# Performance work log

Hardware: AMD Instinct MI355X
Metric: run time of the kernel (lower is better)

The kernel has to match this reference:

```python
import jax, jax.numpy as jnp
import numpy as np

NUM_CLASSES = 91
NUM_ANCHORS = 3234
VAR_XY, VAR_WH = 0.1, 0.2
SCORE_THRESH = 0.05
NMS_THRESH = 0.5
PRE_NMS_TOPK = 200  # original default 400; reduced to bound the [C-1,K,K] IoU buffer
MAX_DET = 100
BATCH = 64


def _xyxy_to_cxcywh(b):
    wh = b[..., 2:] - b[..., :2]
    c = b[..., :2] + 0.5 * wh
    return jnp.concatenate([c, wh], axis=-1)


def _pairwise_iou(b):
    # b: [K,4] xyxy -> [K,K] IoU
    lt = jnp.maximum(b[:, None, :2], b[None, :, :2])
    rb = jnp.minimum(b[:, None, 2:], b[None, :, 2:])
    inter = jnp.prod(jnp.clip(rb - lt, 0.0), axis=-1)
    area = jnp.prod(jnp.clip(b[:, 2:] - b[:, :2], 0.0), axis=-1)
    union = area[:, None] + area[None, :] - inter
    return inter / jnp.maximum(union, 1e-9)


def _nms_keep(boxes):
    # boxes [K,4] already sorted by descending score; greedy NMS keep mask [K]
    K = boxes.shape[0]
    iou = _pairwise_iou(jax.lax.stop_gradient(boxes))
    idx = jnp.arange(K)

    def body(i, keep):
        suppress = keep[i] & (iou[i] > NMS_THRESH) & (idx > i)
        return keep & ~suppress

    return jax.lax.fori_loop(0, K, body, jnp.ones((K,), dtype=bool))


def setup_inputs() -> dict:
    key = jax.random.key(0)
    k1, k2, k3, k4 = jax.random.split(key, 4)
    cls_logits = jax.random.normal(k1, (BATCH, NUM_ANCHORS, NUM_CLASSES), dtype=jnp.float32)
    box_reg = jax.random.normal(k2, (BATCH, NUM_ANCHORS, 4), dtype=jnp.float32)
    # valid normalized anchor boxes in xyxy
    cxy = jax.random.uniform(k3, (NUM_ANCHORS, 2), minval=0.05, maxval=0.95)
    wh = jax.random.uniform(k4, (NUM_ANCHORS, 2), minval=0.02, maxval=0.4)
    priors = jnp.concatenate([cxy - wh / 2, cxy + wh / 2], axis=-1).astype(jnp.float32)
    return {"cls_logits": cls_logits, "box_reg": box_reg, "priors": priors}


def reference(cls_logits, box_reg, priors):
    probs = jax.nn.softmax(cls_logits, axis=-1)           # [B,A,C]
    pr_c = _xyxy_to_cxcywh(priors)                        # [A,4]

    def per_image(args):
        loc, p = args                                     # [A,4], [A,C]
        # _decode with variances (0.1, 0.2)
        xy = loc[:, :2] * VAR_XY * pr_c[:, 2:] + pr_c[:, :2]
        wh = jnp.exp(loc[:, 2:] * VAR_WH) * pr_c[:, 2:]
        boxes = jnp.concatenate([xy - wh / 2, xy + wh / 2], axis=-1)  # [A,4]

        scores_c = p[:, 1:].T                             # [C-1, A], skip background
        vals, idx = jax.lax.top_k(scores_c, PRE_NMS_TOPK)  # [C-1,K] sorted desc
        boxes_c = boxes[idx]                              # [C-1,K,4]
        keep = jax.vmap(_nms_keep)(boxes_c)               # [C-1,K]
        valid = vals > SCORE_THRESH
        fscores = jnp.where(keep & valid, vals, 0.0)      # masked-out dets scored 0
        labels = jnp.broadcast_to(
            jnp.arange(1, NUM_CLASSES, dtype=jnp.float32)[:, None], fscores.shape)

        flat_s = fscores.reshape(-1)
        flat_b = boxes_c.reshape(-1, 4)
        flat_l = labels.reshape(-1)
        top_s, top_i = jax.lax.top_k(flat_s, MAX_DET)     # global top-100 by score
        preds = jnp.concatenate(
            [flat_b[top_i], top_s[:, None], flat_l[top_i, None]], axis=-1)  # [100,6]
        return jnp.where(top_s[:, None] > 0, preds, 0.0)  # zero padding rows

    return jax.lax.map(per_image, (box_reg, probs))        # [B,100,6]
```

## Files before the change

kernel.cpp:

```cpp
#include <hip/hip_runtime.h>
#include <cstdint>

#define NCLS 91
#define NA   3234
#define NB   64
#define KTOP 200
#define CAP  128
#define MAXDET 100
#define NCM1 90
#define CAPI 8192
#define LCAP 256
#define NBIN 1024
#define BOFF 0x3D4C
#define FBUF 1024
#define PBLK 6468

typedef unsigned long long u64;
typedef unsigned int u32;


__device__ __forceinline__ u64 u64max(u64 a, u64 b) { return a > b ? a : b; }
__device__ __forceinline__ u64 u64min(u64 a, u64 b) { return a < b ? a : b; }

__device__ __forceinline__ u64 shfl_xor_u64(u64 v, int m) {
  int lo = __shfl_xor((int)(u32)v, m, 64);
  int hi = __shfl_xor((int)(u32)(v >> 32), m, 64);
  return ((u64)(u32)hi << 32) | (u32)lo;
}

template <int SLOTS>
__device__ __forceinline__ void bitonic_desc(u64* key, int t) {
  const int N = SLOTS * 64;
  for (int k = 2; k <= N; k <<= 1) {
    for (int j = k >> 1; j > 0; j >>= 1) {
      if (j >= 64) {
        int sj = j >> 6;
        #pragma unroll
        for (int s = 0; s < SLOTS; ++s) {
          int sp = s ^ sj;
          if (sp > s) {
            int e = s * 64 + t;
            bool up = ((e & k) == 0);
            u64 a = key[s], b = key[sp];
            u64 mx = u64max(a, b), mn = u64min(a, b);
            key[s]  = up ? mx : mn;
            key[sp] = up ? mn : mx;
          }
        }
      } else {
        #pragma unroll
        for (int s = 0; s < SLOTS; ++s) {
          int e = s * 64 + t;
          u64 p = shfl_xor_u64(key[s], j);
          bool up = ((e & k) == 0);
          bool lower = ((t & j) == 0);
          key[s] = (up == lower) ? u64max(key[s], p) : u64min(key[s], p);
        }
      }
    }
  }
}

__device__ __forceinline__ void process_slab(
    const float* sl, int slab, int t,
    u64* lkey, unsigned short* lbc, int* lcnt) {
  int half = t & 1;
  int r = t >> 1;
  int i = slab * 32 + r;
  int b = i / NA, a = i - b * NA;

  int F0 = half ? 45 : 0;
  int cntf = half ? 46 : 45;
  const float* base = sl + r * 91 + F0;
  int g0 = (int)((u32)(r * 91 + F0) & 3u);
  int lead = (4 - g0) & 3;
  int rem = cntf - lead;
  int n4 = rem >> 2;
  int tail = rem & 3;

  float lv0 = 0.f, lv1 = 0.f, lv2 = 0.f;
  if (lead > 0) lv0 = base[0];
  if (lead > 1) lv1 = base[1];
  if (lead > 2) lv2 = base[2];
  const float4* cv = (const float4*)(base + lead);
  float4 r4[11];
  #pragma unroll
  for (int v = 0; v < 10; ++v) r4[v] = cv[v];
  r4[10] = make_float4(0.f, 0.f, 0.f, 0.f);
  if (n4 > 10) r4[10] = cv[10];
  int toff = lead + 4 * n4;
  float tv0 = 0.f, tv1 = 0.f, tv2 = 0.f;
  if (tail > 0) tv0 = base[toff];
  if (tail > 1) tv1 = base[toff + 1];
  if (tail > 2) tv2 = base[toff + 2];

  float m = -3.402823466e38f;
  if (lead > 0) m = fmaxf(m, lv0);
  if (lead > 1) m = fmaxf(m, lv1);
  if (lead > 2) m = fmaxf(m, lv2);
  #pragma unroll
  for (int v = 0; v < 10; ++v) {
    float4 q = r4[v];
    m = fmaxf(m, fmaxf(fmaxf(q.x, q.y), fmaxf(q.z, q.w)));
  }
  if (n4 > 10) {
    float4 q = r4[10];
    m = fmaxf(m, fmaxf(fmaxf(q.x, q.y), fmaxf(q.z, q.w)));
  }
  if (tail > 0) m = fmaxf(m, tv0);
  if (tail > 1) m = fmaxf(m, tv1);
  if (tail > 2) m = fmaxf(m, tv2);
  m = fmaxf(m, __shfl_xor(m, 1, 64));

  float el0 = expf(lv0 - m), el1 = expf(lv1 - m), el2 = expf(lv2 - m);
  float4 er[11];
  #pragma unroll
  for (int v = 0; v < 11; ++v) {
    er[v].x = expf(r4[v].x - m);
    er[v].y = expf(r4[v].y - m);
    er[v].z = expf(r4[v].z - m);
    er[v].w = expf(r4[v].w - m);
  }
  float et0 = expf(tv0 - m), et1 = expf(tv1 - m), et2 = expf(tv2 - m);

  auto CHAIN = [&](float s) -> float {
    if (lead > 0) s += el0;
    if (lead > 1) s += el1;
    if (lead > 2) s += el2;
    #pragma unroll
    for (int v = 0; v < 10; ++v) {
      s += er[v].x; s += er[v].y; s += er[v].z; s += er[v].w;
    }
    if (n4 > 10) { s += er[10].x; s += er[10].y; s += er[10].z; s += er[10].w; }
    if (tail > 0) s += et0;
    if (tail > 1) s += et1;
    if (tail > 2) s += et2;
    return s;
  };
  float s = 0.f;
  if (!half) s = CHAIN(0.f);
  float s_recv = __shfl_xor(s, 1, 64);
  if (half) s = CHAIN(s_recv);
  float fin = __shfl_xor(s, 1, 64);
  float ssum = half ? s : fin;

  float lthr = logf(0.05f * ssum);
  u64 abits = (u64)(u32)(~a);
  int bb90 = b * NCM1;
  #define PUSH(L, E, CC) do { \
    if ((L) - m > lthr) { \
      float _e = (E); \
      int _lp = atomicAdd(lcnt, 1); \
      if (_lp < LCAP) { \
        lkey[_lp] = ((u64)__float_as_uint(_e / ssum) << 32) | abits; \
        lbc[_lp] = (unsigned short)(bb90 + (CC) - 1); \
      } \
    } \
  } while (0)

  if (lead > 0 && F0 != 0) PUSH(lv0, el0, F0);
  if (lead > 1) PUSH(lv1, el1, F0 + 1);
  if (lead > 2) PUSH(lv2, el2, F0 + 2);
  {
    int c0 = F0 + lead;
    if (c0 != 0) PUSH(r4[0].x, er[0].x, c0);
    PUSH(r4[0].y, er[0].y, c0 + 1);
    PUSH(r4[0].z, er[0].z, c0 + 2);
    PUSH(r4[0].w, er[0].w, c0 + 3);
  }
  #pragma unroll
  for (int v = 1; v < 10; ++v) {
    int cb = F0 + lead + 4 * v;
    PUSH(r4[v].x, er[v].x, cb);
    PUSH(r4[v].y, er[v].y, cb + 1);
    PUSH(r4[v].z, er[v].z, cb + 2);
    PUSH(r4[v].w, er[v].w, cb + 3);
  }
  if (n4 > 10) {
    int cb = F0 + lead + 40;
    PUSH(r4[10].x, er[10].x, cb);
    PUSH(r4[10].y, er[10].y, cb + 1);
    PUSH(r4[10].z, er[10].z, cb + 2);
    PUSH(r4[10].w, er[10].w, cb + 3);
  }
  {
    int cb = F0 + toff;
    if (tail > 0) PUSH(tv0, et0, cb);
    if (tail > 1) PUSH(tv1, et1, cb + 1);
    if (tail > 2) PUSH(tv2, et2, cb + 2);
  }
  #undef PUSH
}

__global__ __launch_bounds__(64, 2) void prep_kernel(
    const float* __restrict__ logits, const float* __restrict__ box_reg,
    const float* __restrict__ priors, float* __restrict__ boxes,
    u64* __restrict__ cand, int* __restrict__ cnt) {
  __shared__ __align__(16) float sl[2912];
  __shared__ u64 lkey[LCAP];
  __shared__ unsigned short lbc[LCAP];
  __shared__ int lcnt;
  int t = threadIdx.x;
  if (t == 0) lcnt = 0;
  asm volatile("s_waitcnt lgkmcnt(0)" ::: "memory");

  int half = t & 1;
  int rloc = t >> 1;
  int i = blockIdx.x * 32 + rloc;
  int b = i / NA, a = i - b * NA;

  float4 pr = make_float4(0.f, 0.f, 0.f, 0.f);
  float4 lc = make_float4(0.f, 0.f, 0.f, 0.f);
  if (!half) {
    pr = ((const float4*)priors)[a];
    lc = ((const float4*)box_reg)[i];
  }

  const float4* gs = (const float4*)(logits + (size_t)blockIdx.x * 2912);
  float4 v0  = gs[0 * 64 + t];
  float4 v1  = gs[1 * 64 + t];
  float4 v2  = gs[2 * 64 + t];
  float4 v3  = gs[3 * 64 + t];
  float4 v4  = gs[4 * 64 + t];
  float4 v5  = gs[5 * 64 + t];
  float4 v6  = gs[6 * 64 + t];
  float4 v7  = gs[7 * 64 + t];
  float4 v8  = gs[8 * 64 + t];
  float4 v9  = gs[9 * 64 + t];
  float4 v10 = gs[10 * 64 + t];
  bool lastl = (t < 24);
  float4 v11 = make_float4(0.f, 0.f, 0.f, 0.f);
  if (lastl) v11 = gs[11 * 64 + t];

  if (!half) {
    float pw = pr.z - pr.x, ph = pr.w - pr.y;
    float cx = pr.x + 0.5f * pw, cy = pr.y + 0.5f * ph;
    float x = lc.x * 0.1f * pw + cx;
    float y = lc.y * 0.1f * ph + cy;
    float bw = expf(lc.z * 0.2f) * pw;
    float bh = expf(lc.w * 0.2f) * ph;
    float4 bxo;
    bxo.x = x - bw * 0.5f; bxo.y = y - bh * 0.5f;
    bxo.z = x + bw * 0.5f; bxo.w = y + bh * 0.5f;
    ((float4*)boxes)[i] = bxo;
  }

  float4* sl4 = (float4*)sl;
  sl4[0 * 64 + t]  = v0;
  sl4[1 * 64 + t]  = v1;
  sl4[2 * 64 + t]  = v2;
  sl4[3 * 64 + t]  = v3;
  sl4[4 * 64 + t]  = v4;
  sl4[5 * 64 + t]  = v5;
  sl4[6 * 64 + t]  = v6;
  sl4[7 * 64 + t]  = v7;
  sl4[8 * 64 + t]  = v8;
  sl4[9 * 64 + t]  = v9;
  sl4[10 * 64 + t] = v10;
  if (lastl) sl4[11 * 64 + t] = v11;

  asm volatile("s_waitcnt lgkmcnt(0)" ::: "memory");
  __builtin_amdgcn_sched_barrier(0);

  process_slab(sl, blockIdx.x, t, lkey, lbc, &lcnt);

  asm volatile("s_waitcnt lgkmcnt(0)" ::: "memory");
  __builtin_amdgcn_sched_barrier(0);
  int nL = lcnt; if (nL > LCAP) nL = LCAP;
  for (int j = t; j < nL; j += 64) {
    int bcv = lbc[j];
    int pos = atomicAdd(&cnt[bcv], 1);
    if (pos < CAP) cand[(size_t)bcv * CAP + pos] = lkey[j];
  }
}

__global__ __launch_bounds__(256) void sort_nms_kernel(
    const u64* __restrict__ cand, const int* __restrict__ cnt,
    const float* __restrict__ boxes,
    u64* __restrict__ img_keys, int* __restrict__ img_cnt) {
  int w = threadIdx.x >> 6;
  int t = threadIdx.x & 63;
  int bc = blockIdx.x * 4 + w;
  int b = bc / NCM1;
  int cm1 = bc - b * NCM1;

  int n = cnt[bc]; if (n > CAP) n = CAP;

  u64 key[2];
  #pragma unroll
  for (int s = 0; s < 2; ++s) {
    int e = s * 64 + t;
    key[s] = (e < n) ? cand[(size_t)bc * CAP + e] : 0ULL;
  }
  if (n <= 64) bitonic_desc<1>(key, t);
  else         bitonic_desc<2>(key, t);

  float4 bx0 = make_float4(0.f, 0.f, 0.f, 0.f);
  float4 bx1 = make_float4(0.f, 0.f, 0.f, 0.f);
  float ar0 = 0.f, ar1 = 0.f;
  if (t < n) {
    int a = (int)(~(u32)key[0]);
    bx0 = ((const float4*)boxes)[b * NA + a];
    ar0 = fmaxf(bx0.z - bx0.x, 0.f) * fmaxf(bx0.w - bx0.y, 0.f);
  }
  if (64 + t < n) {
    int a = (int)(~(u32)key[1]);
    bx1 = ((const float4*)boxes)[b * NA + a];
    ar1 = fmaxf(bx1.z - bx1.x, 0.f) * fmaxf(bx1.w - bx1.y, 0.f);
  }

  auto rng = [](int mm, int wd) -> u64 {
    int c = mm - wd * 64;
    if (c <= 0) return 0ull;
    if (c >= 64) return ~0ull;
    return (1ull << c) - 1ull;
  };
  u64 kp0 = rng(n, 0), kp1 = rng(n, 1);
  bool has1 = (n > 64);

  for (int i = 0; i < n; ++i) {
    bool hi = i >= 64;
    u64 kw = hi ? kp1 : kp0;
    if (!((kw >> (i & 63)) & 1ull)) continue;
    int src = i & 63;
    float bix = __shfl(hi ? bx1.x : bx0.x, src, 64);
    float biy = __shfl(hi ? bx1.y : bx0.y, src, 64);
    float biz = __shfl(hi ? bx1.z : bx0.z, src, 64);
    float biw = __shfl(hi ? bx1.w : bx0.w, src, 64);
    float ai  = __shfl(hi ? ar1 : ar0, src, 64);
    if (!hi) {
      float xx1 = fmaxf(bix, bx0.x), yy1 = fmaxf(biy, bx0.y);
      float xx2 = fminf(biz, bx0.z), yy2 = fminf(biw, bx0.w);
      float inter = fmaxf(xx2 - xx1, 0.f) * fmaxf(yy2 - yy1, 0.f);
      float iou = inter / fmaxf(ai + ar0 - inter, 1e-9f);
      u64 sup0 = __ballot(iou > 0.5f);
      kp0 &= ~(sup0 & ~((2ull << i) - 1ull));
      if (has1) {
        float xx1b = fmaxf(bix, bx1.x), yy1b = fmaxf(biy, bx1.y);
        float xx2b = fminf(biz, bx1.z), yy2b = fminf(biw, bx1.w);
        float interb = fmaxf(xx2b - xx1b, 0.f) * fmaxf(yy2b - yy1b, 0.f);
        float ioub = interb / fmaxf(ai + ar1 - interb, 1e-9f);
        u64 sup1 = __ballot(ioub > 0.5f);
        kp1 &= ~sup1;
      }
    } else {
      float xx1b = fmaxf(bix, bx1.x), yy1b = fmaxf(biy, bx1.y);
      float xx2b = fminf(biz, bx1.z), yy2b = fminf(biw, bx1.w);
      float interb = fmaxf(xx2b - xx1b, 0.f) * fmaxf(yy2b - yy1b, 0.f);
      float ioub = interb / fmaxf(ai + ar1 - interb, 1e-9f);
      u64 sup1 = __ballot(ioub > 0.5f);
      kp1 &= ~(sup1 & ~((2ull << (i - 64)) - 1ull));
    }
  }

  u64 k0 = kp0, k1 = kp1;
  int c0 = __popcll(k0), c1 = __popcll(k1);
  int tot = c0 + c1;
  int base = 0;
  if (t == 0 && tot) base = atomicAdd(&img_cnt[b], tot);
  base = __shfl(base, 0, 64);
  if (tot) {
    u64 lmlt = (1ull << t) - 1ull;
    u64 kws[2] = {k0, k1};
    int pres[2] = {0, c0};
    #pragma unroll
    for (int s = 0; s < 2; ++s) {
      int rr = s * 64 + t;
      if (rr < n && ((kws[s] >> t) & 1ull)) {
        int pos = base + pres[s] + __popcll(kws[s] & lmlt);
        if (pos < CAPI) {
          u32 sbits = (u32)(key[s] >> 32);
          int fidx = cm1 * KTOP + rr;
          int anch = (int)(~(u32)key[s]);
          img_keys[(size_t)b * CAPI + pos] =
              ((u64)sbits << 27) | ((u64)(u32)(0x7FFF - fidx) << 12) | (u64)(u32)anch;
        }
      }
    }
  }
}

__global__ __launch_bounds__(1024) void topdet_kernel(
    const u64* __restrict__ img_keys, const int* __restrict__ img_cnt,
    const float* __restrict__ boxes, float* __restrict__ out) {
  __shared__ int hist[NBIN];
  __shared__ u64 buf[FBUF];
  __shared__ int sh_nsel, sh_T;
  int b = blockIdx.x, t = threadIdx.x;
  int n = img_cnt[b]; if (n > CAPI) n = CAPI;

  for (int i = t; i < NBIN; i += 1024) hist[i] = 0;
  if (t == 0) { sh_nsel = 0; sh_T = 0; }
  __syncthreads();

  for (int i = t; i < n; i += 1024) {
    int bin = (int)(img_keys[(size_t)b * CAPI + i] >> 43) - BOFF;
    bin = bin < 0 ? 0 : (bin > NBIN - 1 ? NBIN - 1 : bin);
    atomicAdd(&hist[bin], 1);
  }
  __syncthreads();

  if (t < 64) {
    int hi = NBIN - 1 - (t << 4);
    int cs = 0;
    #pragma unroll
    for (int k = 0; k < 16; ++k) cs += hist[hi - k];
    int cum = cs;
    for (int d = 1; d < 64; d <<= 1) {
      int o = __shfl_up(cum, d, 64);
      if (t >= d) cum += o;
    }
    int pre = cum - cs;
    if (pre < MAXDET && cum >= MAXDET) {
      int acc = pre;
      for (int k = 0; k < 16; ++k) {
        acc += hist[hi - k];
        if (acc >= MAXDET) { sh_T = hi - k; break; }
      }
    }
  }
  __syncthreads();

  int T = sh_T;
  for (int i = t; i < n; i += 1024) {
    u64 key = img_keys[(size_t)b * CAPI + i];
    int bin = (int)(key >> 43) - BOFF;
    bin = bin < 0 ? 0 : (bin > NBIN - 1 ? NBIN - 1 : bin);
    if (bin >= T) {
      int pos = atomicAdd(&sh_nsel, 1);
      if (pos < FBUF) buf[pos] = key;
    }
  }
  __syncthreads();

  int ns = sh_nsel; if (ns > FBUF) ns = FBUF;

  if (ns <= 256) {
    if (t < 64) {
      u64 key[4];
      #pragma unroll
      for (int s = 0; s < 4; ++s) {
        int e = s * 64 + t;
        key[s] = (e < ns) ? buf[e] : 0ULL;
      }
      if (ns <= 128) bitonic_desc<2>(key, t);
      else           bitonic_desc<4>(key, t);
      buf[t] = key[0];
      if (t < 36) buf[64 + t] = key[1];
    }
    __syncthreads();
  } else {
    int npow = 1; while (npow < ns) npow <<= 1;
    for (int i = t; i < npow; i += 1024) if (i >= ns) buf[i] = 0ULL;
    __syncthreads();
    for (int k = 2; k <= npow; k <<= 1) {
      for (int j = k >> 1; j > 0; j >>= 1) {
        for (int i = t; i < npow; i += 1024) {
          int l = i ^ j;
          if (l > i) {
            u64 x0 = buf[i], x1 = buf[l];
            bool up = ((i & k) == 0);
            if (up ? (x0 < x1) : (x0 > x1)) { buf[i] = x1; buf[l] = x0; }
          }
        }
        __syncthreads();
      }
    }
  }

  if (t < MAXDET) {
    float* row = out + ((size_t)b * MAXDET + t) * 6;
    if (t < ns) {
      u64 key = buf[t];
      float vsc = __uint_as_float((u32)(key >> 27));
      int fidx = 0x7FFF - (int)((key >> 12) & 0x7FFF);
      int a = (int)(key & 0xFFF);
      float4 bb = ((const float4*)boxes)[b * NA + a];
      row[0] = bb.x; row[1] = bb.y; row[2] = bb.z; row[3] = bb.w;
      row[4] = vsc;
      row[5] = (float)(fidx / KTOP + 1);
    } else {
      row[0] = 0.f; row[1] = 0.f; row[2] = 0.f;
      row[3] = 0.f; row[4] = 0.f; row[5] = 0.f;
    }
  }
}

extern "C" void kernel_launch(void* const* d_in, const int* in_sizes, int n_in,
                              void* d_out, int out_size, void* d_ws, size_t ws_size,
                              hipStream_t stream) {
  const float* logits  = (const float*)d_in[0];
  const float* box_reg = (const float*)d_in[1];
  const float* priors  = (const float*)d_in[2];
  float* out = (float*)d_out;

  char* ws = (char*)d_ws;
  size_t off = 0;
  float* boxes = (float*)(ws + off);               off += (size_t)NB * NA * 4 * sizeof(float);
  u64* cand = (u64*)(ws + off);                    off += (size_t)NB * NCM1 * CAP * sizeof(u64);
  u64* img_keys = (u64*)(ws + off);                off += (size_t)NB * CAPI * sizeof(u64);
  int* cnt = (int*)(ws + off);                     off += (size_t)NB * NCM1 * sizeof(int);
  int* img_cnt = (int*)(ws + off);                 off += (size_t)NB * sizeof(int);
  (void)ws_size; (void)in_sizes; (void)n_in; (void)out_size;

  hipMemsetAsync(cnt, 0, (size_t)(NB * NCM1 + NB) * sizeof(int), stream);
  prep_kernel<<<PBLK, 64, 0, stream>>>(
      logits, box_reg, priors, boxes, cand, cnt);
  sort_nms_kernel<<<NB * NCM1 / 4, 256, 0, stream>>>(
      cand, cnt, boxes, img_keys, img_cnt);
  topdet_kernel<<<NB, 1024, 0, stream>>>(img_keys, img_cnt, boxes, out);
}
```

Baseline: 227.2 us.

## Fuse per-class sort/NMS and top-detection into one per-image kernel

Merges the sort+NMS kernel and the top-100 selection kernel into a single kernel with one 1024-thread block per image. Each of the 16 waves handles classes in rounds and writes surviving keys into shared memory (64KB skeys) instead of a global img_keys buffer. This removes a launch, the global atomic counter and the global round-trip. In exchange, the NMS work runs on only 64 blocks with about 6 serial rounds per wave instead of 1440 blocks, and the large shared footprint limits occupancy.

```diff
diff --git a/kernel.cpp b/kernel.cpp
--- a/kernel.cpp
+++ b/kernel.cpp
@@ -274,141 +274,140 @@
   }
 }
 
-__global__ __launch_bounds__(256) void sort_nms_kernel(
+__global__ __launch_bounds__(1024) void finish_kernel(
     const u64* __restrict__ cand, const int* __restrict__ cnt,
-    const float* __restrict__ boxes,
-    u64* __restrict__ img_keys, int* __restrict__ img_cnt) {
-  int w = threadIdx.x >> 6;
-  int t = threadIdx.x & 63;
-  int bc = blockIdx.x * 4 + w;
-  int b = bc / NCM1;
-  int cm1 = bc - b * NCM1;
-
-  int n = cnt[bc]; if (n > CAP) n = CAP;
-
-  u64 key[2];
-  #pragma unroll
-  for (int s = 0; s < 2; ++s) {
-    int e = s * 64 + t;
-    key[s] = (e < n) ? cand[(size_t)bc * CAP + e] : 0ULL;
-  }
-  if (n <= 64) bitonic_desc<1>(key, t);
-  else         bitonic_desc<2>(key, t);
-
-  float4 bx0 = make_float4(0.f, 0.f, 0.f, 0.f);
-  float4 bx1 = make_float4(0.f, 0.f, 0.f, 0.f);
-  float ar0 = 0.f, ar1 = 0.f;
-  if (t < n) {
-    int a = (int)(~(u32)key[0]);
-    bx0 = ((const float4*)boxes)[b * NA + a];
-    ar0 = fmaxf(bx0.z - bx0.x, 0.f) * fmaxf(bx0.w - bx0.y, 0.f);
-  }
-  if (64 + t < n) {
-    int a = (int)(~(u32)key[1]);
-    bx1 = ((const float4*)boxes)[b * NA + a];
-    ar1 = fmaxf(bx1.z - bx1.x, 0.f) * fmaxf(bx1.w - bx1.y, 0.f);
-  }
-
-  auto rng = [](int mm, int wd) -> u64 {
-    int c = mm - wd * 64;
-    if (c <= 0) return 0ull;
-    if (c >= 64) return ~0ull;
-    return (1ull << c) - 1ull;
-  };
-  u64 kp0 = rng(n, 0), kp1 = rng(n, 1);
-  bool has1 = (n > 64);
-
-  for (int i = 0; i < n; ++i) {
-    bool hi = i >= 64;
-    u64 kw = hi ? kp1 : kp0;
-    if (!((kw >> (i & 63)) & 1ull)) continue;
-    int src = i & 63;
-    float bix = __shfl(hi ? bx1.x : bx0.x, src, 64);
-    float biy = __shfl(hi ? bx1.y : bx0.y, src, 64);
-    float biz = __shfl(hi ? bx1.z : bx0.z, src, 64);
-    float biw = __shfl(hi ? bx1.w : bx0.w, src, 64);
-    float ai  = __shfl(hi ? ar1 : ar0, src, 64);
-    if (!hi) {
-      float xx1 = fmaxf(bix, bx0.x), yy1 = fmaxf(biy, bx0.y);
-      float xx2 = fminf(biz, bx0.z), yy2 = fminf(biw, bx0.w);
-      float inter = fmaxf(xx2 - xx1, 0.f) * fmaxf(yy2 - yy1, 0.f);
-      float iou = inter / fmaxf(ai + ar0 - inter, 1e-9f);
-      u64 sup0 = __ballot(iou > 0.5f);
-      kp0 &= ~(sup0 & ~((2ull << i) - 1ull));
-      if (has1) {
-        float xx1b = fmaxf(bix, bx1.x), yy1b = fmaxf(biy, bx1.y);
-        float xx2b = fminf(biz, bx1.z), yy2b = fminf(biw, bx1.w);
-        float interb = fmaxf(xx2b - xx1b, 0.f) * fmaxf(yy2b - yy1b, 0.f);
-        float ioub = interb / fmaxf(ai + ar1 - interb, 1e-9f);
-        u64 sup1 = __ballot(ioub > 0.5f);
-        kp1 &= ~sup1;
-      }
-    } else {
-      float xx1b = fmaxf(bix, bx1.x), yy1b = fmaxf(biy, bx1.y);
-      float xx2b = fminf(biz, bx1.z), yy2b = fminf(biw, bx1.w);
-      float interb = fmaxf(xx2b - xx1b, 0.f) * fmaxf(yy2b - yy1b, 0.f);
-      float ioub = interb / fmaxf(ai + ar1 - interb, 1e-9f);
-      u64 sup1 = __ballot(ioub > 0.5f);
-      kp1 &= ~(sup1 & ~((2ull << (i - 64)) - 1ull));
-    }
-  }
-
-  u64 k0 = kp0, k1 = kp1;
-  int c0 = __popcll(k0), c1 = __popcll(k1);
-  int tot = c0 + c1;
-  int base = 0;
-  if (t == 0 && tot) base = atomicAdd(&img_cnt[b], tot);
-  base = __shfl(base, 0, 64);
-  if (tot) {
-    u64 lmlt = (1ull << t) - 1ull;
-    u64 kws[2] = {k0, k1};
-    int pres[2] = {0, c0};
-    #pragma unroll
-    for (int s = 0; s < 2; ++s) {
-      int rr = s * 64 + t;
-      if (rr < n && ((kws[s] >> t) & 1ull)) {
-        int pos = base + pres[s] + __popcll(kws[s] & lmlt);
-        if (pos < CAPI) {
-          u32 sbits = (u32)(key[s] >> 32);
-          int fidx = cm1 * KTOP + rr;
-          int anch = (int)(~(u32)key[s]);
-          img_keys[(size_t)b * CAPI + pos] =
-              ((u64)sbits << 27) | ((u64)(u32)(0x7FFF - fidx) << 12) | (u64)(u32)anch;
-        }
-      }
-    }
-  }
-}
-
-__global__ __launch_bounds__(1024) void topdet_kernel(
-    const u64* __restrict__ img_keys, const int* __restrict__ img_cnt,
     const float* __restrict__ boxes, float* __restrict__ out) {
+  __shared__ u64 skeys[CAPI];
   __shared__ int hist[NBIN];
   __shared__ u64 buf[FBUF];
-  __shared__ int sh_nsel, sh_T;
-  int b = blockIdx.x, t = threadIdx.x;
-  int n = img_cnt[b]; if (n > CAPI) n = CAPI;
-
-  for (int i = t; i < NBIN; i += 1024) hist[i] = 0;
-  if (t == 0) { sh_nsel = 0; sh_T = 0; }
+  __shared__ int scnt, sh_nsel, sh_T;
+  int b = blockIdx.x;
+  int tid = threadIdx.x;
+  int w = tid >> 6;
+  int t = tid & 63;
+  for (int i = tid; i < NBIN; i += 1024) hist[i] = 0;
+  if (tid == 0) { scnt = 0; sh_nsel = 0; sh_T = 0; }
   __syncthreads();
 
-  for (int i = t; i < n; i += 1024) {
-    int bin = (int)(img_keys[(size_t)b * CAPI + i] >> 43) - BOFF;
+  for (int rnd = 0; rnd < 6; ++rnd) {
+    int cm1 = rnd * 16 + w;
+    if (cm1 < NCM1) {
+      int bc = b * NCM1 + cm1;
+      int n = cnt[bc]; if (n > CAP) n = CAP;
+
+      u64 key[2];
+      #pragma unroll
+      for (int s = 0; s < 2; ++s) {
+        int e = s * 64 + t;
+        key[s] = (e < n) ? cand[(size_t)bc * CAP + e] : 0ULL;
+      }
+      if (n <= 64) bitonic_desc<1>(key, t);
+      else         bitonic_desc<2>(key, t);
+
+      float4 bx0 = make_float4(0.f, 0.f, 0.f, 0.f);
+      float4 bx1 = make_float4(0.f, 0.f, 0.f, 0.f);
+      float ar0 = 0.f, ar1 = 0.f;
+      if (t < n) {
+        int a = (int)(~(u32)key[0]);
+        bx0 = ((const float4*)boxes)[b * NA + a];
+        ar0 = fmaxf(bx0.z - bx0.x, 0.f) * fmaxf(bx0.w - bx0.y, 0.f);
+      }
+      if (64 + t < n) {
+        int a = (int)(~(u32)key[1]);
+        bx1 = ((const float4*)boxes)[b * NA + a];
+        ar1 = fmaxf(bx1.z - bx1.x, 0.f) * fmaxf(bx1.w - bx1.y, 0.f);
+      }
+
+      auto rng = [](int mm, int wd) -> u64 {
+        int c = mm - wd * 64;
+        if (c <= 0) return 0ull;
+        if (c >= 64) return ~0ull;
+        return (1ull << c) - 1ull;
+      };
+      u64 kp0 = rng(n, 0), kp1 = rng(n, 1);
+      bool has1 = (n > 64);
+
+      for (int i = 0; i < n; ++i) {
+        bool hi = i >= 64;
+        u64 kw = hi ? kp1 : kp0;
+        if (!((kw >> (i & 63)) & 1ull)) continue;
+        int src = i & 63;
+        float bix = __shfl(hi ? bx1.x : bx0.x, src, 64);
+        float biy = __shfl(hi ? bx1.y : bx0.y, src, 64);
+        float biz = __shfl(hi ? bx1.z : bx0.z, src, 64);
+        float biw = __shfl(hi ? bx1.w : bx0.w, src, 64);
+        float ai  = __shfl(hi ? ar1 : ar0, src, 64);
+        if (!hi) {
+          float xx1 = fmaxf(bix, bx0.x), yy1 = fmaxf(biy, bx0.y);
+          float xx2 = fminf(biz, bx0.z), yy2 = fminf(biw, bx0.w);
+          float inter = fmaxf(xx2 - xx1, 0.f) * fmaxf(yy2 - yy1, 0.f);
+          float iou = inter / fmaxf(ai + ar0 - inter, 1e-9f);
+          u64 sup0 = __ballot(iou > 0.5f);
+          kp0 &= ~(sup0 & ~((2ull << i) - 1ull));
+          if (has1) {
+            float xx1b = fmaxf(bix, bx1.x), yy1b = fmaxf(biy, bx1.y);
+            float xx2b = fminf(biz, bx1.z), yy2b = fminf(biw, bx1.w);
+            float interb = fmaxf(xx2b - xx1b, 0.f) * fmaxf(yy2b - yy1b, 0.f);
+            float ioub = interb / fmaxf(ai + ar1 - interb, 1e-9f);
+            u64 sup1 = __ballot(ioub > 0.5f);
+            kp1 &= ~sup1;
+          }
+        } else {
+          float xx1b = fmaxf(bix, bx1.x), yy1b = fmaxf(biy, bx1.y);
+          float xx2b = fminf(biz, bx1.z), yy2b = fminf(biw, bx1.w);
+          float interb = fmaxf(xx2b - xx1b, 0.f) * fmaxf(yy2b - yy1b, 0.f);
+          float ioub = interb / fmaxf(ai + ar1 - interb, 1e-9f);
+          u64 sup1 = __ballot(ioub > 0.5f);
+          kp1 &= ~(sup1 & ~((2ull << (i - 64)) - 1ull));
+        }
+      }
+
+      int c0 = __popcll(kp0), c1 = __popcll(kp1);
+      int tot = c0 + c1;
+      int base = 0;
+      if (t == 0 && tot) base = atomicAdd(&scnt, tot);
+      base = __shfl(base, 0, 64);
+      if (tot) {
+        u64 lmlt = (1ull << t) - 1ull;
+        u64 kws[2] = {kp0, kp1};
+        int pres[2] = {0, c0};
+        #pragma unroll
+        for (int s = 0; s < 2; ++s) {
+          int rr = s * 64 + t;
+          if (rr < n && ((kws[s] >> t) & 1ull)) {
+            int pos = base + pres[s] + __popcll(kws[s] & lmlt);
+            if (pos < CAPI) {
+              u32 sbits = (u32)(key[s] >> 32);
+              int fidx = cm1 * KTOP + rr;
+              int anch = (int)(~(u32)key[s]);
+              skeys[pos] =
+                  ((u64)sbits << 27) | ((u64)(u32)(0x7FFF - fidx) << 12) | (u64)(u32)anch;
+            }
+          }
+        }
+      }
+    }
+  }
+  __syncthreads();
+
+  int n = scnt; if (n > CAPI) n = CAPI;
+
+  for (int i = tid; i < n; i += 1024) {
+    int bin = (int)(skeys[i] >> 43) - BOFF;
     bin = bin < 0 ? 0 : (bin > NBIN - 1 ? NBIN - 1 : bin);
     atomicAdd(&hist[bin], 1);
   }
   __syncthreads();
 
-  if (t < 64) {
-    int hi = NBIN - 1 - (t << 4);
+  if (tid < 64) {
+    int hi = NBIN - 1 - (tid << 4);
     int cs = 0;
     #pragma unroll
     for (int k = 0; k < 16; ++k) cs += hist[hi - k];
     int cum = cs;
     for (int d = 1; d < 64; d <<= 1) {
       int o = __shfl_up(cum, d, 64);
-      if (t >= d) cum += o;
+      if (tid >= d) cum += o;
     }
     int pre = cum - cs;
     if (pre < MAXDET && cum >= MAXDET) {
@@ -422,8 +421,8 @@
   __syncthreads();
 
   int T = sh_T;
-  for (int i = t; i < n; i += 1024) {
-    u64 key = img_keys[(size_t)b * CAPI + i];
+  for (int i = tid; i < n; i += 1024) {
+    u64 key = skeys[i];
     int bin = (int)(key >> 43) - BOFF;
     bin = bin < 0 ? 0 : (bin > NBIN - 1 ? NBIN - 1 : bin);
     if (bin >= T) {
@@ -436,26 +435,26 @@
   int ns = sh_nsel; if (ns > FBUF) ns = FBUF;
 
   if (ns <= 256) {
-    if (t < 64) {
+    if (tid < 64) {
       u64 key[4];
       #pragma unroll
       for (int s = 0; s < 4; ++s) {
-        int e = s * 64 + t;
+        int e = s * 64 + tid;
         key[s] = (e < ns) ? buf[e] : 0ULL;
       }
-      if (ns <= 128) bitonic_desc<2>(key, t);
-      else           bitonic_desc<4>(key, t);
-      buf[t] = key[0];
-      if (t < 36) buf[64 + t] = key[1];
+      if (ns <= 128) bitonic_desc<2>(key, tid);
+      else           bitonic_desc<4>(key, tid);
+      buf[tid] = key[0];
+      if (tid < 36) buf[64 + tid] = key[1];
     }
     __syncthreads();
   } else {
     int npow = 1; while (npow < ns) npow <<= 1;
-    for (int i = t; i < npow; i += 1024) if (i >= ns) buf[i] = 0ULL;
+    for (int i = tid; i < npow; i += 1024) if (i >= ns) buf[i] = 0ULL;
     __syncthreads();
     for (int k = 2; k <= npow; k <<= 1) {
       for (int j = k >> 1; j > 0; j >>= 1) {
-        for (int i = t; i < npow; i += 1024) {
+        for (int i = tid; i < npow; i += 1024) {
           int l = i ^ j;
           if (l > i) {
             u64 x0 = buf[i], x1 = buf[l];
@@ -468,10 +467,10 @@
     }
   }
 
-  if (t < MAXDET) {
-    float* row = out + ((size_t)b * MAXDET + t) * 6;
-    if (t < ns) {
-      u64 key = buf[t];
+  if (tid < MAXDET) {
+    float* row = out + ((size_t)b * MAXDET + tid) * 6;
+    if (tid < ns) {
+      u64 key = buf[tid];
       float vsc = __uint_as_float((u32)(key >> 27));
       int fidx = 0x7FFF - (int)((key >> 12) & 0x7FFF);
       int a = (int)(key & 0xFFF);
@@ -498,15 +497,11 @@
   size_t off = 0;
   float* boxes = (float*)(ws + off);               off += (size_t)NB * NA * 4 * sizeof(float);
   u64* cand = (u64*)(ws + off);                    off += (size_t)NB * NCM1 * CAP * sizeof(u64);
-  u64* img_keys = (u64*)(ws + off);                off += (size_t)NB * CAPI * sizeof(u64);
   int* cnt = (int*)(ws + off);                     off += (size_t)NB * NCM1 * sizeof(int);
-  int* img_cnt = (int*)(ws + off);                 off += (size_t)NB * sizeof(int);
   (void)ws_size; (void)in_sizes; (void)n_in; (void)out_size;
 
-  hipMemsetAsync(cnt, 0, (size_t)(NB * NCM1 + NB) * sizeof(int), stream);
+  hipMemsetAsync(cnt, 0, (size_t)(NB * NCM1) * sizeof(int), stream);
   prep_kernel<<<PBLK, 64, 0, stream>>>(
       logits, box_reg, priors, boxes, cand, cnt);
-  sort_nms_kernel<<<NB * NCM1 / 4, 256, 0, stream>>>(
-      cand, cnt, boxes, img_keys, img_cnt);
-  topdet_kernel<<<NB, 1024, 0, stream>>>(img_keys, img_cnt, boxes, out);
+  finish_kernel<<<NB, 1024, 0, stream>>>(cand, cnt, boxes, out);
 }
```

After: 390.8 us. +72.0%, slower.
